# Performance work log

Measured on AMD Instinct MI355X. Metric: run time of the kernel, lower is better.

The kernel has to match this reference:

```python
import jax, jax.numpy as jnp
import numpy as np

BATCH, SEQ, NFEAT, HID = 128, 2048, 64, 256


def setup_inputs() -> dict:
    key = jax.random.key(0)
    ks = jax.random.split(key, 9)
    k = 1.0 / np.sqrt(HID)  # PyTorch LSTM/Linear init range
    u = lambda kk, shp: jax.random.uniform(kk, shp, jnp.float32, -k, k)
    return {
        "ts_batch": jax.random.normal(ks[0], (BATCH, SEQ, NFEAT), jnp.float32),
        "Wih_e": u(ks[1], (4 * HID, NFEAT)),
        "Whh_e": u(ks[2], (4 * HID, HID)),
        "b_e": u(ks[3], (4 * HID,)),  # b_ih + b_hh combined
        "Wih_d": u(ks[4], (4 * HID, NFEAT)),
        "Whh_d": u(ks[5], (4 * HID, HID)),
        "b_d": u(ks[6], (4 * HID,)),
        "Wout": u(ks[7], (NFEAT, HID)),
        "bout": u(ks[8], (NFEAT,)),
    }


def _lstm_cell(x, h, c, Wih, Whh, b):
    # gates: [B, 4H], PyTorch order (i, f, g, o)
    gates = x @ Wih.T + h @ Whh.T + b
    i, f, g, o = jnp.split(gates, 4, axis=-1)
    c_new = jax.nn.sigmoid(f) * c + jax.nn.sigmoid(i) * jnp.tanh(g)
    h_new = jax.nn.sigmoid(o) * jnp.tanh(c_new)
    return h_new, c_new


def reference(ts_batch, Wih_e, Whh_e, b_e, Wih_d, Whh_d, b_d, Wout, bout):
    B, T, F = ts_batch.shape
    H = Whh_e.shape[1]
    h0 = jnp.zeros((B, H), ts_batch.dtype)
    c0 = jnp.zeros((B, H), ts_batch.dtype)

    xs = jnp.swapaxes(ts_batch, 0, 1)  # [T, B, F]

    def enc_step(carry, x):
        h, c = carry
        h, c = _lstm_cell(x, h, c, Wih_e, Whh_e, b_e)
        return (h, c), None

    enc_hc, _ = jax.lax.scan(enc_step, (h0, c0), xs)

    # Decoder (training branch): for i = T-1 .. 0:
    #   output[:, i] = Linear(h)  (before update)
    #   h, c = LSTMCell(ts_batch[:, i], h, c)
    def dec_step(carry, x):
        h, c = carry
        out = h @ Wout.T + bout  # [B, F]
        h, c = _lstm_cell(x, h, c, Wih_d, Whh_d, b_d)
        return (h, c), out

    _, outs_rev = jax.lax.scan(dec_step, enc_hc, xs[::-1])
    return jnp.swapaxes(outs_rev[::-1], 0, 1)  # [B, T, F]
```

## Files before the change

### kernel.cpp

```cpp
#include <hip/hip_runtime.h>

#define TT 2048
#define FF 64
#define HH 256
#define ZSTR 328

typedef short short8 __attribute__((ext_vector_type(8)));
typedef float f32x4 __attribute__((ext_vector_type(4)));
typedef unsigned long long u64t;
typedef unsigned u32t;

#define WS_HB_B 1343488

__device__ inline unsigned short f2b(float f) {
  unsigned int u = __builtin_bit_cast(unsigned int, f);
  u += 0x7fffu + ((u >> 16) & 1u);
  return (unsigned short)(u >> 16);
}
__device__ inline u32t pk2(float a, float b) {
  return (u32t)f2b(a) | ((u32t)f2b(b) << 16);
}

__global__ void prep_kernel(const float* __restrict__ Wih_e, const float* __restrict__ Whh_e,
                            const float* __restrict__ Wih_d, const float* __restrict__ Whh_d,
                            const float* __restrict__ Wout, unsigned short* __restrict__ ws) {
  int idx = blockIdx.x * blockDim.x + threadIdx.x;
  if (idx >= 83968) return;
  const float* src; unsigned short* dst; int q, kdim;
  if (idx < 32768)      { q = idx;         src = Whh_e; dst = ws + 0      + q * 8; kdim = HH; }
  else if (idx < 40960) { q = idx - 32768; src = Wih_e; dst = ws + 262144 + q * 8; kdim = FF; }
  else if (idx < 73728) { q = idx - 40960; src = Whh_d; dst = ws + 327680 + q * 8; kdim = HH; }
  else if (idx < 81920) { q = idx - 73728; src = Wih_d; dst = ws + 589824 + q * 8; kdim = FF; }
  else                  { q = idx - 81920; src = Wout;  dst = ws + 655360 + q * 8; kdim = HH; }
  int ksPerTile = (kdim == HH) ? 8 : 2;
  int per = ksPerTile * 64;
  int tile = q / per, rem = q % per;
  int ks = rem / 64, l = rem % 64;
  int col = tile * 16 + (l & 15);
  int k0 = ks * 32 + (l >> 4) * 8;
#pragma unroll
  for (int e = 0; e < 8; e++) dst[e] = f2b(src[col * kdim + k0 + e]);
}

__global__ void init_hb(u64t* __restrict__ hb) {
  int i = blockIdx.x * blockDim.x + threadIdx.x;
  if (i < 32768) hb[i] = 0ull;
}

__global__ __launch_bounds__(256, 1) void lstm_kernel(
    const float* __restrict__ xg, const float* __restrict__ b_e,
    const float* __restrict__ b_d, const float* __restrict__ bout,
    const unsigned short* __restrict__ wsu, float* __restrict__ out,
    u64t* __restrict__ hb) {
  extern __shared__ unsigned short smem[];
  unsigned short* zbb      = smem;
  unsigned short* wout_lds = smem + 10496;
  unsigned short* whh_lds  = smem + 14592;

  const int tid = threadIdx.x;
  const int l = tid & 63, w = tid >> 6;
  const int ln = l & 15, lk = l >> 4;
  const int bb = blockIdx.x & 7, gg = blockIdx.x >> 3;
  const int b0 = bb * 16;

  const int U = 64 * gg + 16 * w + ln;
  const float bo_ = bout[16 * gg + ln];

  {
    const short8* WoutP = (const short8*)(wsu + 655360);
    short8* wl = (short8*)wout_lds;
    wl[tid] = WoutP[gg * 512 + tid];
    wl[tid + 256] = WoutP[gg * 512 + tid + 256];
  }

  int cidx[6], crow[6], cU[6];
#pragma unroll
  for (int k = 0; k < 6; k++) {
    int m = k * 256 + tid;
    int pu = m >> 3, rp = m & 7;
    int Up = pu + (pu >= 64 * gg ? 64 : 0);
    cidx[k] = (bb * 256 + Up) * 8 + rp;
    crow[k] = 2 * rp;
    cU[k] = Up;
  }
  const int p0 = (bb * 256 + U) * 8 + 2 * lk;

  float creg[4] = {0.f, 0.f, 0.f, 0.f};

  const int xrow = tid >> 4, xf = (tid & 15) * 4;
  const float* xrp = xg + (size_t)(b0 + xrow) * TT * FF + xf;
  float4 xv = *(const float4*)xrp;

#pragma unroll
  for (int i = 0; i < 8; i++) {
    int q = i * 256 + tid;
    *(u32t*)&zbb[(q >> 7) * ZSTR + (q & 127) * 2] = 0u;
  }
  *(u32t*)&zbb[xrow * ZSTR + HH + xf]     = pk2(xv.x, xv.y);
  *(u32t*)&zbb[xrow * ZSTR + HH + xf + 2] = pk2(xv.z, xv.w);
  xv = *(const float4*)(xrp + FF);

  for (int ph = 0; ph < 2; ++ph) {
    const short8* WhhP = (const short8*)(wsu + (ph ? 327680 : 0));
    const short8* WihP = (const short8*)(wsu + (ph ? 589824 : 262144));
    const float* bias = ph ? b_d : b_e;

    __syncthreads();
    {
      short8* wl = (short8*)whh_lds;
#pragma unroll
      for (int k = 0; k < 32; k++) {
        int i = tid + 256 * k;
        int lane = i & 63, ks = (i >> 6) & 7, tl = i >> 9;
        int c = (tl >> 2) * 16 + 4 * gg + (tl & 3);
        wl[i] = WhhP[(c * 8 + ks) * 64 + lane];
      }
    }
    float bact[4];
#pragma unroll
    for (int g = 0; g < 4; g++) bact[g] = bias[g * 256 + U];
    __syncthreads();

    const short8* WH = (const short8*)whh_lds;
    short8 rB[4][8];
#pragma unroll
    for (int g = 0; g < 4; g++)
#pragma unroll
      for (int ks = 0; ks < 8; ks++)
        rB[g][ks] = WH[((g * 4 + w) * 8 + ks) * 64 + l];
    short8 rX[4][2];
#pragma unroll
    for (int g = 0; g < 4; g++)
#pragma unroll
      for (int j = 0; j < 2; j++)
        rX[g][j] = WihP[((g * 16 + 4 * gg + w) * 2 + j) * 64 + l];

#pragma unroll 1
    for (int ti = 0; ti < TT; ++ti) {
      const int it = ph * TT + ti;
      const int t = ph ? (TT - 1 - ti) : ti;
      unsigned short* zc = zbb + (it & 1) * (16 * ZSTR);
      unsigned short* zn = zbb + ((it & 1) ^ 1) * (16 * ZSTR);

      short8 aX0 = *(const short8*)&zc[ln * ZSTR + 256 + lk * 8];
      short8 aX1 = *(const short8*)&zc[ln * ZSTR + 288 + lk * 8];
      f32x4 acc[4];
#pragma unroll
      for (int g = 0; g < 4; g++) {
        acc[g] = f32x4{0.f, 0.f, 0.f, 0.f};
        acc[g] = __builtin_amdgcn_mfma_f32_16x16x32_bf16(aX0, rX[g][0], acc[g], 0, 0, 0);
        acc[g] = __builtin_amdgcn_mfma_f32_16x16x32_bf16(aX1, rX[g][1], acc[g], 0, 0, 0);
      }

      if (it) {
        const u64t* base = hb + (size_t)(it & 1) * 16384;
        u64t v0 = 0, v1 = 0, v2 = 0, v3 = 0, v4 = 0, v5 = 0;
        bool d0 = false, d1 = false, d2 = false, d3 = false, d4 = false, d5 = false;
        do {
          if (!d0) { v0 = __hip_atomic_load(base + cidx[0], __ATOMIC_RELAXED, __HIP_MEMORY_SCOPE_AGENT);
                     d0 = ((u32t)v0 == (u32t)it); }
          if (!d1) { v1 = __hip_atomic_load(base + cidx[1], __ATOMIC_RELAXED, __HIP_MEMORY_SCOPE_AGENT);
                     d1 = ((u32t)v1 == (u32t)it); }
          if (!d2) { v2 = __hip_atomic_load(base + cidx[2], __ATOMIC_RELAXED, __HIP_MEMORY_SCOPE_AGENT);
                     d2 = ((u32t)v2 == (u32t)it); }
          if (!d3) { v3 = __hip_atomic_load(base + cidx[3], __ATOMIC_RELAXED, __HIP_MEMORY_SCOPE_AGENT);
                     d3 = ((u32t)v3 == (u32t)it); }
          if (!d4) { v4 = __hip_atomic_load(base + cidx[4], __ATOMIC_RELAXED, __HIP_MEMORY_SCOPE_AGENT);
                     d4 = ((u32t)v4 == (u32t)it); }
          if (!d5) { v5 = __hip_atomic_load(base + cidx[5], __ATOMIC_RELAXED, __HIP_MEMORY_SCOPE_AGENT);
                     d5 = ((u32t)v5 == (u32t)it); }
        } while (!(d0 && d1 && d2 && d3 && d4 && d5));
        zc[crow[0] * ZSTR + cU[0]] = (unsigned short)(v0 >> 32);
        zc[(crow[0] + 1) * ZSTR + cU[0]] = (unsigned short)(v0 >> 48);
        zc[crow[1] * ZSTR + cU[1]] = (unsigned short)(v1 >> 32);
        zc[(crow[1] + 1) * ZSTR + cU[1]] = (unsigned short)(v1 >> 48);
        zc[crow[2] * ZSTR + cU[2]] = (unsigned short)(v2 >> 32);
        zc[(crow[2] + 1) * ZSTR + cU[2]] = (unsigned short)(v2 >> 48);
        zc[crow[3] * ZSTR + cU[3]] = (unsigned short)(v3 >> 32);
        zc[(crow[3] + 1) * ZSTR + cU[3]] = (unsigned short)(v3 >> 48);
        zc[crow[4] * ZSTR + cU[4]] = (unsigned short)(v4 >> 32);
        zc[(crow[4] + 1) * ZSTR + cU[4]] = (unsigned short)(v4 >> 48);
        zc[crow[5] * ZSTR + cU[5]] = (unsigned short)(v5 >> 32);
        zc[(crow[5] + 1) * ZSTR + cU[5]] = (unsigned short)(v5 >> 48);
      }
      __syncthreads();

      short8 afr[8];
#pragma unroll
      for (int ks = 0; ks < 8; ks++)
        afr[ks] = *(const short8*)&zc[ln * ZSTR + ks * 32 + lk * 8];
#pragma unroll
      for (int ks = 0; ks < 8; ks++)
#pragma unroll
        for (int g = 0; g < 4; g++)
          acc[g] = __builtin_amdgcn_mfma_f32_16x16x32_bf16(afr[ks], rB[g][ks], acc[g], 0, 0, 0);

      unsigned short hu[4];
#pragma unroll
      for (int r = 0; r < 4; r++) {
        float gi = acc[0][r] + bact[0];
        float gf = acc[1][r] + bact[1];
        float gG = acc[2][r] + bact[2];
        float go = acc[3][r] + bact[3];
        float si = 1.f / (1.f + __expf(-gi));
        float sf = 1.f / (1.f + __expf(-gf));
        float tg = 1.f - 2.f / (__expf(2.f * gG) + 1.f);
        float so = 1.f / (1.f + __expf(-go));
        float cn = sf * creg[r] + si * tg;
        creg[r] = cn;
        float hn = so * (1.f - 2.f / (__expf(2.f * cn) + 1.f));
        hu[r] = f2b(hn);
      }

      {
        u64t* bp = hb + (size_t)((it + 1) & 1) * 16384;
        const u64t tag = (u64t)(u32t)(it + 1);
        __hip_atomic_store(bp + p0,     tag | ((u64t)((u32t)hu[0] | ((u32t)hu[1] << 16)) << 32),
                           __ATOMIC_RELAXED, __HIP_MEMORY_SCOPE_AGENT);
        __hip_atomic_store(bp + p0 + 1, tag | ((u64t)((u32t)hu[2] | ((u32t)hu[3] << 16)) << 32),
                           __ATOMIC_RELAXED, __HIP_MEMORY_SCOPE_AGENT);
      }

      zn[(4 * lk + 0) * ZSTR + U] = hu[0];
      zn[(4 * lk + 1) * ZSTR + U] = hu[1];
      zn[(4 * lk + 2) * ZSTR + U] = hu[2];
      zn[(4 * lk + 3) * ZSTR + U] = hu[3];

      if (ph == 1 && w == (ti & 3)) {
        const short8* WO = (const short8*)wout_lds;
        f32x4 oa = {0.f, 0.f, 0.f, 0.f};
#pragma unroll
        for (int ks = 0; ks < 8; ks++)
          oa = __builtin_amdgcn_mfma_f32_16x16x32_bf16(afr[ks], WO[ks * 64 + l], oa, 0, 0, 0);
#pragma unroll
        for (int r = 0; r < 4; r++)
          out[((size_t)(b0 + 4 * lk + r) * TT + t) * FF + 16 * gg + ln] = oa[r] + bo_;
      }

      *(u32t*)&zn[xrow * ZSTR + HH + xf]     = pk2(xv.x, xv.y);
      *(u32t*)&zn[xrow * ZSTR + HH + xf + 2] = pk2(xv.z, xv.w);
      {
        int it2 = it + 2; if (it2 >= 2 * TT) it2 = 0;
        int t2 = (it2 < TT) ? it2 : (2 * TT - 1 - it2);
        xv = *(const float4*)(xrp + (size_t)t2 * FF);
      }
      __syncthreads();
    }
  }
}

extern "C" void kernel_launch(void* const* d_in, const int* in_sizes, int n_in,
                              void* d_out, int out_size, void* d_ws, size_t ws_size,
                              hipStream_t stream) {
  const float* ts    = (const float*)d_in[0];
  const float* Wih_e = (const float*)d_in[1];
  const float* Whh_e = (const float*)d_in[2];
  const float* b_e   = (const float*)d_in[3];
  const float* Wih_d = (const float*)d_in[4];
  const float* Whh_d = (const float*)d_in[5];
  const float* b_d   = (const float*)d_in[6];
  const float* Wout  = (const float*)d_in[7];
  const float* bout  = (const float*)d_in[8];
  unsigned short* ws = (unsigned short*)d_ws;
  float* out = (float*)d_out;
  u64t* hb = (u64t*)((char*)d_ws + WS_HB_B);

  const int ldsBytes = (10496 + 4096 + 65536) * 2;
  (void)hipFuncSetAttribute((const void*)lstm_kernel,
                            hipFuncAttributeMaxDynamicSharedMemorySize, ldsBytes);

  prep_kernel<<<328, 256, 0, stream>>>(Wih_e, Whh_e, Wih_d, Whh_d, Wout, ws);
  init_hb<<<64, 512, 0, stream>>>(hb);
  lstm_kernel<<<32, 256, ldsBytes, stream>>>(ts, b_e, b_d, bout, ws, out, hb);
}
```

Before: 11.39 ms.

## Use single LDS z-buffer and move x-projection MFMAs after spin-wait

Replaces the double-buffered z tile in LDS with a single buffer. Each step first writes its own h and x into the buffer, then waits on peers, syncs, reads all A fragments (including x) into registers, and syncs again before computing. The x-projection MFMAs now run after the wait together with the recurrent MFMAs, and the x prefetch distance drops from two steps to one. This shrinks LDS use and changes the barrier layout, but the input-projection work no longer overlaps the spin-wait and is now on the critical path.

```diff
diff --git a/kernel.cpp b/kernel.cpp
--- a/kernel.cpp
+++ b/kernel.cpp
@@ -53,9 +53,9 @@
     const unsigned short* __restrict__ wsu, float* __restrict__ out,
     u64t* __restrict__ hb) {
   extern __shared__ unsigned short smem[];
-  unsigned short* zbb      = smem;
-  unsigned short* wout_lds = smem + 10496;
-  unsigned short* whh_lds  = smem + 14592;
+  unsigned short* zb       = smem;
+  unsigned short* wout_lds = smem + 5248;
+  unsigned short* whh_lds  = smem + 9344;
 
   const int tid = threadIdx.x;
   const int l = tid & 63, w = tid >> 6;
@@ -86,6 +86,7 @@
   const int p0 = (bb * 256 + U) * 8 + 2 * lk;
 
   float creg[4] = {0.f, 0.f, 0.f, 0.f};
+  unsigned short hu[4] = {0, 0, 0, 0};
 
   const int xrow = tid >> 4, xf = (tid & 15) * 4;
   const float* xrp = xg + (size_t)(b0 + xrow) * TT * FF + xf;
@@ -94,11 +95,8 @@
 #pragma unroll
   for (int i = 0; i < 8; i++) {
     int q = i * 256 + tid;
-    *(u32t*)&zbb[(q >> 7) * ZSTR + (q & 127) * 2] = 0u;
-  }
-  *(u32t*)&zbb[xrow * ZSTR + HH + xf]     = pk2(xv.x, xv.y);
-  *(u32t*)&zbb[xrow * ZSTR + HH + xf + 2] = pk2(xv.z, xv.w);
-  xv = *(const float4*)(xrp + FF);
+    *(u32t*)&zb[(q >> 7) * ZSTR + (q & 127) * 2] = 0u;
+  }
 
   for (int ph = 0; ph < 2; ++ph) {
     const short8* WhhP = (const short8*)(wsu + (ph ? 327680 : 0));
@@ -122,12 +120,12 @@
     __syncthreads();
 
     const short8* WH = (const short8*)whh_lds;
-    short8 rB[4][8];
+    short8 rW[4][8];
 #pragma unroll
     for (int g = 0; g < 4; g++)
 #pragma unroll
       for (int ks = 0; ks < 8; ks++)
-        rB[g][ks] = WH[((g * 4 + w) * 8 + ks) * 64 + l];
+        rW[g][ks] = WH[((g * 4 + w) * 8 + ks) * 64 + l];
     short8 rX[4][2];
 #pragma unroll
     for (int g = 0; g < 4; g++)
@@ -139,18 +137,13 @@
     for (int ti = 0; ti < TT; ++ti) {
       const int it = ph * TT + ti;
       const int t = ph ? (TT - 1 - ti) : ti;
-      unsigned short* zc = zbb + (it & 1) * (16 * ZSTR);
-      unsigned short* zn = zbb + ((it & 1) ^ 1) * (16 * ZSTR);
-
-      short8 aX0 = *(const short8*)&zc[ln * ZSTR + 256 + lk * 8];
-      short8 aX1 = *(const short8*)&zc[ln * ZSTR + 288 + lk * 8];
-      f32x4 acc[4];
-#pragma unroll
-      for (int g = 0; g < 4; g++) {
-        acc[g] = f32x4{0.f, 0.f, 0.f, 0.f};
-        acc[g] = __builtin_amdgcn_mfma_f32_16x16x32_bf16(aX0, rX[g][0], acc[g], 0, 0, 0);
-        acc[g] = __builtin_amdgcn_mfma_f32_16x16x32_bf16(aX1, rX[g][1], acc[g], 0, 0, 0);
-      }
+
+      *(u32t*)&zb[xrow * ZSTR + HH + xf]     = pk2(xv.x, xv.y);
+      *(u32t*)&zb[xrow * ZSTR + HH + xf + 2] = pk2(xv.z, xv.w);
+      zb[(4 * lk + 0) * ZSTR + U] = hu[0];
+      zb[(4 * lk + 1) * ZSTR + U] = hu[1];
+      zb[(4 * lk + 2) * ZSTR + U] = hu[2];
+      zb[(4 * lk + 3) * ZSTR + U] = hu[3];
 
       if (it) {
         const u64t* base = hb + (size_t)(it & 1) * 16384;
@@ -170,32 +163,49 @@
           if (!d5) { v5 = __hip_atomic_load(base + cidx[5], __ATOMIC_RELAXED, __HIP_MEMORY_SCOPE_AGENT);
                      d5 = ((u32t)v5 == (u32t)it); }
         } while (!(d0 && d1 && d2 && d3 && d4 && d5));
-        zc[crow[0] * ZSTR + cU[0]] = (unsigned short)(v0 >> 32);
-        zc[(crow[0] + 1) * ZSTR + cU[0]] = (unsigned short)(v0 >> 48);
-        zc[crow[1] * ZSTR + cU[1]] = (unsigned short)(v1 >> 32);
-        zc[(crow[1] + 1) * ZSTR + cU[1]] = (unsigned short)(v1 >> 48);
-        zc[crow[2] * ZSTR + cU[2]] = (unsigned short)(v2 >> 32);
-        zc[(crow[2] + 1) * ZSTR + cU[2]] = (unsigned short)(v2 >> 48);
-        zc[crow[3] * ZSTR + cU[3]] = (unsigned short)(v3 >> 32);
-        zc[(crow[3] + 1) * ZSTR + cU[3]] = (unsigned short)(v3 >> 48);
-        zc[crow[4] * ZSTR + cU[4]] = (unsigned short)(v4 >> 32);
-        zc[(crow[4] + 1) * ZSTR + cU[4]] = (unsigned short)(v4 >> 48);
-        zc[crow[5] * ZSTR + cU[5]] = (unsigned short)(v5 >> 32);
-        zc[(crow[5] + 1) * ZSTR + cU[5]] = (unsigned short)(v5 >> 48);
+        zb[crow[0] * ZSTR + cU[0]] = (unsigned short)(v0 >> 32);
+        zb[(crow[0] + 1) * ZSTR + cU[0]] = (unsigned short)(v0 >> 48);
+        zb[crow[1] * ZSTR + cU[1]] = (unsigned short)(v1 >> 32);
+        zb[(crow[1] + 1) * ZSTR + cU[1]] = (unsigned short)(v1 >> 48);
+        zb[crow[2] * ZSTR + cU[2]] = (unsigned short)(v2 >> 32);
+        zb[(crow[2] + 1) * ZSTR + cU[2]] = (unsigned short)(v2 >> 48);
+        zb[crow[3] * ZSTR + cU[3]] = (unsigned short)(v3 >> 32);
+        zb[(crow[3] + 1) * ZSTR + cU[3]] = (unsigned short)(v3 >> 48);
+        zb[crow[4] * ZSTR + cU[4]] = (unsigned short)(v4 >> 32);
+        zb[(crow[4] + 1) * ZSTR + cU[4]] = (unsigned short)(v4 >> 48);
+        zb[crow[5] * ZSTR + cU[5]] = (unsigned short)(v5 >> 32);
+        zb[(crow[5] + 1) * ZSTR + cU[5]] = (unsigned short)(v5 >> 48);
       }
       __syncthreads();
 
-      short8 afr[8];
+      short8 afr[10];
 #pragma unroll
       for (int ks = 0; ks < 8; ks++)
-        afr[ks] = *(const short8*)&zc[ln * ZSTR + ks * 32 + lk * 8];
+        afr[ks] = *(const short8*)&zb[ln * ZSTR + ks * 32 + lk * 8];
+      afr[8] = *(const short8*)&zb[ln * ZSTR + 256 + lk * 8];
+      afr[9] = *(const short8*)&zb[ln * ZSTR + 288 + lk * 8];
+      __syncthreads();
+
+      {
+        int it2 = it + 1; if (it2 >= 2 * TT) it2 = 0;
+        int t2 = (it2 < TT) ? it2 : (2 * TT - 1 - it2);
+        xv = *(const float4*)(xrp + (size_t)t2 * FF);
+      }
+
+      f32x4 acc[4];
+#pragma unroll
+      for (int g = 0; g < 4; g++) acc[g] = f32x4{0.f, 0.f, 0.f, 0.f};
 #pragma unroll
       for (int ks = 0; ks < 8; ks++)
 #pragma unroll
         for (int g = 0; g < 4; g++)
-          acc[g] = __builtin_amdgcn_mfma_f32_16x16x32_bf16(afr[ks], rB[g][ks], acc[g], 0, 0, 0);
-
-      unsigned short hu[4];
+          acc[g] = __builtin_amdgcn_mfma_f32_16x16x32_bf16(afr[ks], rW[g][ks], acc[g], 0, 0, 0);
+#pragma unroll
+      for (int j = 0; j < 2; j++)
+#pragma unroll
+        for (int g = 0; g < 4; g++)
+          acc[g] = __builtin_amdgcn_mfma_f32_16x16x32_bf16(afr[8 + j], rX[g][j], acc[g], 0, 0, 0);
+
 #pragma unroll
       for (int r = 0; r < 4; r++) {
         float gi = acc[0][r] + bact[0];
@@ -221,11 +231,6 @@
                            __ATOMIC_RELAXED, __HIP_MEMORY_SCOPE_AGENT);
       }
 
-      zn[(4 * lk + 0) * ZSTR + U] = hu[0];
-      zn[(4 * lk + 1) * ZSTR + U] = hu[1];
-      zn[(4 * lk + 2) * ZSTR + U] = hu[2];
-      zn[(4 * lk + 3) * ZSTR + U] = hu[3];
-
       if (ph == 1 && w == (ti & 3)) {
         const short8* WO = (const short8*)wout_lds;
         f32x4 oa = {0.f, 0.f, 0.f, 0.f};
@@ -236,15 +241,6 @@
         for (int r = 0; r < 4; r++)
           out[((size_t)(b0 + 4 * lk + r) * TT + t) * FF + 16 * gg + ln] = oa[r] + bo_;
       }
-
-      *(u32t*)&zn[xrow * ZSTR + HH + xf]     = pk2(xv.x, xv.y);
-      *(u32t*)&zn[xrow * ZSTR + HH + xf + 2] = pk2(xv.z, xv.w);
-      {
-        int it2 = it + 2; if (it2 >= 2 * TT) it2 = 0;
-        int t2 = (it2 < TT) ? it2 : (2 * TT - 1 - it2);
-        xv = *(const float4*)(xrp + (size_t)t2 * FF);
-      }
-      __syncthreads();
     }
   }
 }
@@ -265,7 +261,7 @@
   float* out = (float*)d_out;
   u64t* hb = (u64t*)((char*)d_ws + WS_HB_B);
 
-  const int ldsBytes = (10496 + 4096 + 65536) * 2;
+  const int ldsBytes = (5248 + 4096 + 65536) * 2;
   (void)hipFuncSetAttribute((const void*)lstm_kernel,
                             hipFuncAttributeMaxDynamicSharedMemorySize, ldsBytes);
 
```

Measured after the change: 12.23 ms. 7.4% more time.
